# Kernel optimization log

Measured on AMD Instinct MI355X. Metric: run time of the kernel, lower is better.

## Reference

```python
import jax, jax.numpy as jnp
import numpy as np
from jax import lax

WIRES = 4
EPS = 1e-5


def _conv2d(x, w, b):
    # x: [B,C,H,W], w: [O,I,3,3], SAME padding, stride 1
    y = lax.conv_general_dilated(x, w, (1, 1), 'SAME',
                                 dimension_numbers=('NCHW', 'OIHW', 'NCHW'))
    return y + b[None, :, None, None]


def _maxpool2(x):
    return lax.reduce_window(x, -jnp.inf, lax.max, (1, 1, 2, 2), (1, 1, 2, 2), 'VALID')


def _cnot_perm(c, t, n=WIRES):
    # wire 0 = most significant bit; CNOT is a self-inverse basis permutation
    idx = np.arange(2 ** n)
    cbit = (idx >> (n - 1 - c)) & 1
    flipped = idx ^ (1 << (n - 1 - t))
    return np.where(cbit == 1, flipped, idx)


_CNOT_PERMS = [_cnot_perm(c, c + 1) for c in range(WIRES - 1)]
_Z_SIGNS = np.stack([1.0 - 2.0 * ((np.arange(2 ** WIRES) >> (WIRES - 1 - i)) & 1)
                     for i in range(WIRES)], axis=1).astype(np.float32)  # [16, 4]


def _quantum_circuit(q_params, feats):
    # Batched state-vector sim of: RY(feats[i]) wire i; RX(params[i]) wire i;
    # CNOT chain; <Z_i>.  feats: [B,4], q_params: [4]
    hf = 0.5 * feats
    hp = 0.5 * q_params
    cy, sy = jnp.cos(hf), jnp.sin(hf)            # [B,4]
    cx, sx = jnp.cos(hp), jnp.sin(hp)            # [4]
    # per-wire state after RX @ RY |0>: amplitudes of |0>, |1>
    a0 = (cx * cy - 1j * sx * sy).astype(jnp.complex64)  # [B,4]
    a1 = (cx * sy - 1j * sx * cy).astype(jnp.complex64)  # [B,4]
    single = jnp.stack([a0, a1], axis=-1)        # [B,4,2]
    # product state -> full 16-dim state via successive outer products
    psi = single[:, 0]                           # [B,2]
    for i in range(1, WIRES):
        psi = (psi[:, :, None] * single[:, i][:, None, :]).reshape(psi.shape[0], -1)
    # CNOT chain = fixed basis permutations
    for perm in _CNOT_PERMS:
        psi = psi[:, perm]                       # [B,16]
    probs = psi.real ** 2 + psi.imag ** 2        # [B,16]
    return probs @ jnp.asarray(_Z_SIGNS)         # [B,4]


def setup_inputs() -> dict:
    key = jax.random.key(0)
    ks = jax.random.split(key, 8)
    B, C, H, W = 512, 1, 128, 128
    return {
        'x': jax.random.normal(ks[0], (B, C, H, W), jnp.float32),
        'conv1_w': jax.random.normal(ks[1], (8, C, 3, 3), jnp.float32) * 0.1,
        'conv1_b': jnp.zeros((8,), jnp.float32),
        'conv2_w': jax.random.normal(ks[2], (16, 8, 3, 3), jnp.float32) * 0.1,
        'conv2_b': jnp.zeros((16,), jnp.float32),
        'q_params': jax.random.normal(ks[3], (WIRES,), jnp.float32),
        'bn_gamma': jnp.ones((4,), jnp.float32),
        'bn_beta': jnp.zeros((4,), jnp.float32),
        'head_w': jax.random.normal(ks[4], (4, WIRES), jnp.float32) * 0.5,
        'head_b': jnp.zeros((4,), jnp.float32),
    }


def reference(x, conv1_w, conv1_b, conv2_w, conv2_b, q_params,
              bn_gamma, bn_beta, head_w, head_b):
    h = jax.nn.relu(_conv2d(x, conv1_w, conv1_b))
    h = _maxpool2(h)
    h = jax.nn.relu(_conv2d(h, conv2_w, conv2_b))
    h = _maxpool2(h)
    feats = h.mean(axis=(2, 3))                  # AdaptiveAvgPool2d(1) -> [B,16]
    q_out = _quantum_circuit(q_params, feats[:, :WIRES])  # [B,4]
    # BatchNorm1d (training mode, biased variance)
    mu = q_out.mean(axis=0)
    var = q_out.var(axis=0)
    normed = bn_gamma * (q_out - mu) / jnp.sqrt(var + EPS) + bn_beta
    return normed @ head_w.T + head_b
```

## Files before the change

### kernel.cpp

```cpp
#include <hip/hip_runtime.h>

#define EPS 1e-5f

typedef float f2 __attribute__((ext_vector_type(2)));
typedef float f4 __attribute__((ext_vector_type(4)));

__device__ __forceinline__ float uload(const float* __restrict__ p) {
  return __int_as_float(__builtin_amdgcn_readfirstlane(__float_as_int(*p)));
}

__device__ __forceinline__ f2 fma2(f2 a, f2 b, f2 c) {
  return __builtin_elementwise_fma(a, b, c);
}
__device__ __forceinline__ f2 splat2(float s) { f2 r; r.x = s; r.y = s; return r; }

__global__ __launch_bounds__(256, 4) void k12_fused(
    const float* __restrict__ x, const float* __restrict__ w1,
    const float* __restrict__ b1, const float* __restrict__ w2,
    const float* __restrict__ b2, float* __restrict__ partials) {
  __shared__ float p1[4][18][66];
  __shared__ float w1t[72];
  __shared__ float b1s[8];
  __shared__ float w2t[288];
  __shared__ float b2s[4];
  __shared__ float wred[4][4];

  const int q   = blockIdx.x & 3;
  const int b   = blockIdx.x >> 2;
  const int tid = threadIdx.x;
  const float* xb = x + (size_t)b * (128 * 128);

  if (tid < 72) {
    int oc = tid / 9, k = tid % 9;
    w1t[k * 8 + oc] = w1[tid];
  } else if (tid < 80) {
    b1s[tid - 72] = b1[tid - 72];
  } else if (tid < 84) {
    b2s[tid - 80] = b2[tid - 80];
  }
  {
    int t = tid;
    {
      int oc = t / 72, rem = t % 72, ic = rem / 9, k = rem % 9;
      w2t[(ic * 9 + k) * 4 + oc] = w2[t];
    }
    t = tid + 256;
    if (t < 288) {
      int oc = t / 72, rem = t % 72, ic = rem / 9, k = rem % 9;
      w2t[(ic * 9 + k) * 4 + oc] = w2[t];
    }
  }
  if (tid < 72) {
    int ic = tid / 18, r = tid % 18;
    p1[ic][r][0]  = 0.f;
    p1[ic][r][65] = 0.f;
  }
  __syncthreads();

  const int px2  = tid & 31;
  const int py2l = tid >> 5;

  f2 acc[2][2][2];
#pragma unroll
  for (int p = 0; p < 2; ++p) {
    const f2 bias = *(const f2*)&b2s[2 * p];
    acc[p][0][0] = bias; acc[p][0][1] = bias;
    acc[p][1][0] = bias; acc[p][1][1] = bias;
  }

#pragma unroll 1
  for (int g = 0; g < 2; ++g) {
    if (g) __syncthreads();

    f2 wp[9][2], bias1[2];
#pragma unroll
    for (int k = 0; k < 9; ++k) {
      wp[k][0] = *(const f2*)&w1t[k * 8 + 4 * g];
      wp[k][1] = *(const f2*)&w1t[k * 8 + 4 * g + 2];
    }
    bias1[0] = *(const f2*)&b1s[4 * g];
    bias1[1] = *(const f2*)&b1s[4 * g + 2];

#pragma unroll 1
    for (int pos = tid; pos < 576; pos += 256) {
      const int gl = pos >> 5, i = pos & 31;
      const int G  = 16 * q - 1 + gl;
      const bool vG = ((unsigned)G) < 64u;
      const int xr0 = 2 * G - 1;
      float xin[4][6];
#pragma unroll
      for (int r = 0; r < 4; ++r) {
        const int row  = xr0 + r;
        const bool rok = vG && ((unsigned)row < 128u);
        const int rowc = min(max(row, 0), 127);
        const float* rp = xb + rowc * 128;
        const float le = rp[(i == 0) ? 0 : (4 * i - 1)];
        const f4 mid   = *(const f4*)(rp + 4 * i);
        const float ri = rp[(i == 31) ? 127 : (4 * i + 4)];
        xin[r][0] = (rok && i != 0)  ? le    : 0.f;
        xin[r][1] = rok              ? mid.x : 0.f;
        xin[r][2] = rok              ? mid.y : 0.f;
        xin[r][3] = rok              ? mid.z : 0.f;
        xin[r][4] = rok              ? mid.w : 0.f;
        xin[r][5] = (rok && i != 31) ? ri    : 0.f;
      }
      f2 best[2][2];
#pragma unroll
      for (int p = 0; p < 2; ++p)
#pragma unroll
        for (int h = 0; h < 2; ++h) best[p][h] = splat2(0.f);
#pragma unroll
      for (int dy = 0; dy < 2; ++dy)
#pragma unroll
        for (int dx = 0; dx < 2; ++dx) {
#pragma unroll
          for (int p = 0; p < 2; ++p)
#pragma unroll
            for (int h = 0; h < 2; ++h) {
              f2 a = bias1[p];
#pragma unroll
              for (int ky = 0; ky < 3; ++ky)
#pragma unroll
                for (int kx = 0; kx < 3; ++kx)
                  a = fma2(wp[ky * 3 + kx][p],
                           splat2(xin[dy + ky][2 * h + dx + kx]), a);
              best[p][h].x = fmaxf(best[p][h].x, a.x);
              best[p][h].y = fmaxf(best[p][h].y, a.y);
            }
        }
#pragma unroll
      for (int p = 0; p < 2; ++p)
#pragma unroll
        for (int h = 0; h < 2; ++h) {
          p1[2 * p][gl][2 * i + 1 + h]     = vG ? best[p][h].x : 0.f;
          p1[2 * p + 1][gl][2 * i + 1 + h] = vG ? best[p][h].y : 0.f;
        }
    }
    __syncthreads();

#pragma unroll 1
    for (int ic = 0; ic < 4; ++ic) {
      float xin[4][4];
#pragma unroll
      for (int r = 0; r < 4; ++r) {
        const f2* rp = (const f2*)&p1[ic][2 * py2l + r][2 * px2];
        f2 v0 = rp[0], v1 = rp[1];
        xin[r][0] = v0.x; xin[r][1] = v0.y; xin[r][2] = v1.x; xin[r][3] = v1.y;
      }
      const int icg = 4 * g + ic;
#pragma unroll
      for (int ky = 0; ky < 3; ++ky)
#pragma unroll
        for (int kx = 0; kx < 3; ++kx) {
          const int k = ky * 3 + kx;
          const f2 w0 = *(const f2*)&w2t[(icg * 9 + k) * 4];
          const f2 w1p = *(const f2*)&w2t[(icg * 9 + k) * 4 + 2];
#pragma unroll
          for (int dy = 0; dy < 2; ++dy)
#pragma unroll
            for (int dx = 0; dx < 2; ++dx) {
              const f2 xs = splat2(xin[dy + ky][dx + kx]);
              acc[0][dy][dx] = fma2(w0, xs, acc[0][dy][dx]);
              acc[1][dy][dx] = fma2(w1p, xs, acc[1][dy][dx]);
            }
        }
    }
  }

  const int lane = tid & 63, w = tid >> 6;
#pragma unroll
  for (int p = 0; p < 2; ++p) {
    f2 m01;
    m01.x = fmaxf(fmaxf(fmaxf(acc[p][0][0].x, acc[p][0][1].x),
                        fmaxf(acc[p][1][0].x, acc[p][1][1].x)), 0.f);
    m01.y = fmaxf(fmaxf(fmaxf(acc[p][0][0].y, acc[p][0][1].y),
                        fmaxf(acc[p][1][0].y, acc[p][1][1].y)), 0.f);
#pragma unroll
    for (int off = 32; off > 0; off >>= 1) {
      m01.x += __shfl_down(m01.x, off);
      m01.y += __shfl_down(m01.y, off);
    }
    if (lane == 0) { wred[w][2 * p] = m01.x; wred[w][2 * p + 1] = m01.y; }
  }
  __syncthreads();
  if (tid < 4) {
    float s = wred[0][tid] + wred[1][tid] + wred[2][tid] + wred[3][tid];
    partials[((size_t)b * 4 + q) * 4 + tid] = s;
  }
}

__global__ __launch_bounds__(512) void k3_tail(
    const float* __restrict__ partials, const float* __restrict__ qp,
    const float* __restrict__ gamma, const float* __restrict__ beta,
    const float* __restrict__ hw, const float* __restrict__ hb,
    float* __restrict__ out) {
  __shared__ float wsum[8][8];
  __shared__ float stats[8];
  const int tid = threadIdx.x;

  const f4* pp = (const f4*)(partials + tid * 16);
  f4 s0 = pp[0], s1 = pp[1], s2 = pp[2], s3 = pp[3];
  float f[4];
  f[0] = (s0.x + s1.x + s2.x + s3.x) * (1.f / 1024.f);
  f[1] = (s0.y + s1.y + s2.y + s3.y) * (1.f / 1024.f);
  f[2] = (s0.z + s1.z + s2.z + s3.z) * (1.f / 1024.f);
  f[3] = (s0.w + s1.w + s2.w + s3.w) * (1.f / 1024.f);

  float a0r[4], a0i[4], a1r[4], a1i[4];
#pragma unroll
  for (int i = 0; i < 4; ++i) {
    float cy, sy, cx, sx;
    __sincosf(0.5f * f[i], &sy, &cy);
    __sincosf(0.5f * uload(qp + i), &sx, &cx);
    a0r[i] = cx * cy; a0i[i] = -sx * sy;
    a1r[i] = cx * sy; a1i[i] = -sx * cy;
  }

  float pr[16], pi[16];
#pragma unroll
  for (int j = 0; j < 16; ++j) {
    float rr = 1.f, ii = 0.f;
#pragma unroll
    for (int w = 0; w < 4; ++w) {
      int bit = (j >> (3 - w)) & 1;
      float ar = bit ? a1r[w] : a0r[w];
      float ai = bit ? a1i[w] : a0i[w];
      float t = rr * ar - ii * ai;
      ii = rr * ai + ii * ar;
      rr = t;
    }
    pr[j] = rr; pi[j] = ii;
  }

  constexpr int comp[16] = {0, 1, 3, 2, 6, 7, 5, 4, 12, 13, 15, 14, 10, 11, 9, 8};
  float qv[4] = {0.f, 0.f, 0.f, 0.f};
#pragma unroll
  for (int j = 0; j < 16; ++j) {
    int s = comp[j];
    float p = pr[s] * pr[s] + pi[s] * pi[s];
#pragma unroll
    for (int i = 0; i < 4; ++i)
      qv[i] += ((j >> (3 - i)) & 1) ? -p : p;
  }

  float v[8];
#pragma unroll
  for (int i = 0; i < 4; ++i) { v[i] = qv[i]; v[4 + i] = qv[i] * qv[i]; }
#pragma unroll
  for (int k = 0; k < 8; ++k)
#pragma unroll
    for (int off = 32; off > 0; off >>= 1) v[k] += __shfl_down(v[k], off);
  const int lane = tid & 63, w = tid >> 6;
  if (lane == 0) {
#pragma unroll
    for (int k = 0; k < 8; ++k) wsum[w][k] = v[k];
  }
  __syncthreads();
  if (tid < 8) {
    float s = 0.f;
#pragma unroll
    for (int ww = 0; ww < 8; ++ww) s += wsum[ww][tid];
    stats[tid] = s * (1.f / 512.f);
  }
  __syncthreads();

  float nm[4];
#pragma unroll
  for (int i = 0; i < 4; ++i) {
    float mu  = stats[i];
    float var = stats[4 + i] - mu * mu;
    nm[i] = uload(gamma + i) * (qv[i] - mu) * rsqrtf(var + EPS) + uload(beta + i);
  }
#pragma unroll
  for (int k = 0; k < 4; ++k) {
    float o = uload(hb + k);
#pragma unroll
    for (int i = 0; i < 4; ++i) o = fmaf(nm[i], uload(hw + k * 4 + i), o);
    out[tid * 4 + k] = o;
  }
}

extern "C" void kernel_launch(void* const* d_in, const int* in_sizes, int n_in,
                              void* d_out, int out_size, void* d_ws, size_t ws_size,
                              hipStream_t stream) {
  const float* x  = (const float*)d_in[0];
  const float* w1 = (const float*)d_in[1];
  const float* b1 = (const float*)d_in[2];
  const float* w2 = (const float*)d_in[3];
  const float* b2 = (const float*)d_in[4];
  const float* qp = (const float*)d_in[5];
  const float* gm = (const float*)d_in[6];
  const float* bt = (const float*)d_in[7];
  const float* hw = (const float*)d_in[8];
  const float* hb = (const float*)d_in[9];
  float* out = (float*)d_out;

  float* partials = (float*)d_ws;

  k12_fused<<<512 * 4, 256, 0, stream>>>(x, w1, b1, w2, b2, partials);
  k3_tail<<<1, 512, 0, stream>>>(partials, qp, gm, bt, hw, hb, out);
}
```

Before: 123.2 us.

## Compute all eight conv1 channels in one pass, reusing loaded input tile

The kernel now keeps all 8 pooled conv1 channels in shared memory at once, instead of processing two groups of 4 channels with a barrier between them. Each input tile is loaded from global memory once and reused for both channel groups, and one of the __syncthreads is removed. Biases are packed into the weight arrays. In exchange, shared memory per block roughly doubles to about 40 KB, which may lower occupancy below the 4 blocks per CU requested by the launch bounds.

```diff
diff --git a/kernel.cpp b/kernel.cpp
--- a/kernel.cpp
+++ b/kernel.cpp
@@ -18,11 +18,9 @@
     const float* __restrict__ x, const float* __restrict__ w1,
     const float* __restrict__ b1, const float* __restrict__ w2,
     const float* __restrict__ b2, float* __restrict__ partials) {
-  __shared__ float p1[4][18][66];
-  __shared__ float w1t[72];
-  __shared__ float b1s[8];
-  __shared__ float w2t[288];
-  __shared__ float b2s[4];
+  __shared__ float p1[8][18][66];
+  __shared__ float w1t[80];
+  __shared__ float w2t[292];
   __shared__ float wred[4][4];
 
   const int q   = blockIdx.x & 3;
@@ -34,9 +32,7 @@
     int oc = tid / 9, k = tid % 9;
     w1t[k * 8 + oc] = w1[tid];
   } else if (tid < 80) {
-    b1s[tid - 72] = b1[tid - 72];
-  } else if (tid < 84) {
-    b2s[tid - 80] = b2[tid - 80];
+    w1t[tid] = b1[tid - 72];
   }
   {
     int t = tid;
@@ -50,121 +46,111 @@
       w2t[(ic * 9 + k) * 4 + oc] = w2[t];
     }
   }
-  if (tid < 72) {
-    int ic = tid / 18, r = tid % 18;
+  if (tid >= 80 && tid < 84) w2t[288 + tid - 80] = b2[tid - 80];
+  if (tid >= 96 && tid < 240) {
+    int t = tid - 96;
+    int ic = t / 18, r = t % 18;
     p1[ic][r][0]  = 0.f;
     p1[ic][r][65] = 0.f;
   }
   __syncthreads();
 
+#pragma unroll 1
+  for (int pos = tid; pos < 576; pos += 256) {
+    const int gl = pos >> 5, i = pos & 31;
+    const int G  = 16 * q - 1 + gl;
+    const bool vG = ((unsigned)G) < 64u;
+    const int xr0 = 2 * G - 1;
+    float xin[4][6];
+#pragma unroll
+    for (int r = 0; r < 4; ++r) {
+      const int row  = xr0 + r;
+      const bool rok = vG && ((unsigned)row < 128u);
+      const int rowc = min(max(row, 0), 127);
+      const float* rp = xb + rowc * 128;
+      const float le = rp[(i == 0) ? 0 : (4 * i - 1)];
+      const f4 mid   = *(const f4*)(rp + 4 * i);
+      const float ri = rp[(i == 31) ? 127 : (4 * i + 4)];
+      xin[r][0] = (rok && i != 0)  ? le    : 0.f;
+      xin[r][1] = rok              ? mid.x : 0.f;
+      xin[r][2] = rok              ? mid.y : 0.f;
+      xin[r][3] = rok              ? mid.z : 0.f;
+      xin[r][4] = rok              ? mid.w : 0.f;
+      xin[r][5] = (rok && i != 31) ? ri    : 0.f;
+    }
+#pragma unroll 1
+    for (int g = 0; g < 2; ++g) {
+      f2 wpx[9][2], bias1[2];
+#pragma unroll
+      for (int k = 0; k < 9; ++k) {
+        wpx[k][0] = *(const f2*)&w1t[k * 8 + 4 * g];
+        wpx[k][1] = *(const f2*)&w1t[k * 8 + 4 * g + 2];
+      }
+      bias1[0] = *(const f2*)&w1t[72 + 4 * g];
+      bias1[1] = *(const f2*)&w1t[72 + 4 * g + 2];
+#pragma unroll
+      for (int p = 0; p < 2; ++p)
+#pragma unroll
+        for (int h = 0; h < 2; ++h) {
+          f2 best = splat2(0.f);
+#pragma unroll
+          for (int dy = 0; dy < 2; ++dy)
+#pragma unroll
+            for (int dx = 0; dx < 2; ++dx) {
+              f2 a = bias1[p];
+#pragma unroll
+              for (int ky = 0; ky < 3; ++ky)
+#pragma unroll
+                for (int kx = 0; kx < 3; ++kx)
+                  a = fma2(wpx[ky * 3 + kx][p],
+                           splat2(xin[dy + ky][2 * h + dx + kx]), a);
+              best.x = fmaxf(best.x, a.x);
+              best.y = fmaxf(best.y, a.y);
+            }
+          const int oc0 = 4 * g + 2 * p;
+          p1[oc0][gl][2 * i + 1 + h]     = vG ? best.x : 0.f;
+          p1[oc0 + 1][gl][2 * i + 1 + h] = vG ? best.y : 0.f;
+        }
+    }
+  }
+  __syncthreads();
+
   const int px2  = tid & 31;
   const int py2l = tid >> 5;
 
   f2 acc[2][2][2];
 #pragma unroll
   for (int p = 0; p < 2; ++p) {
-    const f2 bias = *(const f2*)&b2s[2 * p];
+    const f2 bias = *(const f2*)&w2t[288 + 2 * p];
     acc[p][0][0] = bias; acc[p][0][1] = bias;
     acc[p][1][0] = bias; acc[p][1][1] = bias;
   }
 
 #pragma unroll 1
-  for (int g = 0; g < 2; ++g) {
-    if (g) __syncthreads();
-
-    f2 wp[9][2], bias1[2];
-#pragma unroll
-    for (int k = 0; k < 9; ++k) {
-      wp[k][0] = *(const f2*)&w1t[k * 8 + 4 * g];
-      wp[k][1] = *(const f2*)&w1t[k * 8 + 4 * g + 2];
-    }
-    bias1[0] = *(const f2*)&b1s[4 * g];
-    bias1[1] = *(const f2*)&b1s[4 * g + 2];
-
-#pragma unroll 1
-    for (int pos = tid; pos < 576; pos += 256) {
-      const int gl = pos >> 5, i = pos & 31;
-      const int G  = 16 * q - 1 + gl;
-      const bool vG = ((unsigned)G) < 64u;
-      const int xr0 = 2 * G - 1;
-      float xin[4][6];
-#pragma unroll
-      for (int r = 0; r < 4; ++r) {
-        const int row  = xr0 + r;
-        const bool rok = vG && ((unsigned)row < 128u);
-        const int rowc = min(max(row, 0), 127);
-        const float* rp = xb + rowc * 128;
-        const float le = rp[(i == 0) ? 0 : (4 * i - 1)];
-        const f4 mid   = *(const f4*)(rp + 4 * i);
-        const float ri = rp[(i == 31) ? 127 : (4 * i + 4)];
-        xin[r][0] = (rok && i != 0)  ? le    : 0.f;
-        xin[r][1] = rok              ? mid.x : 0.f;
-        xin[r][2] = rok              ? mid.y : 0.f;
-        xin[r][3] = rok              ? mid.z : 0.f;
-        xin[r][4] = rok              ? mid.w : 0.f;
-        xin[r][5] = (rok && i != 31) ? ri    : 0.f;
+  for (int ic = 0; ic < 8; ++ic) {
+    float xin[4][4];
+#pragma unroll
+    for (int r = 0; r < 4; ++r) {
+      const f2* rp = (const f2*)&p1[ic][2 * py2l + r][2 * px2];
+      f2 v0 = rp[0], v1 = rp[1];
+      xin[r][0] = v0.x; xin[r][1] = v0.y; xin[r][2] = v1.x; xin[r][3] = v1.y;
+    }
+#pragma unroll
+    for (int ky = 0; ky < 3; ++ky)
+#pragma unroll
+      for (int kx = 0; kx < 3; ++kx) {
+        const int k = ky * 3 + kx;
+        const f2 w0  = *(const f2*)&w2t[(ic * 9 + k) * 4];
+        const f2 w1p = *(const f2*)&w2t[(ic * 9 + k) * 4 + 2];
+#pragma unroll
+        for (int dy = 0; dy < 2; ++dy)
+#pragma unroll
+          for (int dx = 0; dx < 2; ++dx) {
+            const f2 xs = splat2(xin[dy + ky][dx + kx]);
+            acc[0][dy][dx] = fma2(w0, xs, acc[0][dy][dx]);
+            acc[1][dy][dx] = fma2(w1p, xs, acc[1][dy][dx]);
+          }
       }
-      f2 best[2][2];
-#pragma unroll
-      for (int p = 0; p < 2; ++p)
-#pragma unroll
-        for (int h = 0; h < 2; ++h) best[p][h] = splat2(0.f);
-#pragma unroll
-      for (int dy = 0; dy < 2; ++dy)
-#pragma unroll
-        for (int dx = 0; dx < 2; ++dx) {
-#pragma unroll
-          for (int p = 0; p < 2; ++p)
-#pragma unroll
-            for (int h = 0; h < 2; ++h) {
-              f2 a = bias1[p];
-#pragma unroll
-              for (int ky = 0; ky < 3; ++ky)
-#pragma unroll
-                for (int kx = 0; kx < 3; ++kx)
-                  a = fma2(wp[ky * 3 + kx][p],
-                           splat2(xin[dy + ky][2 * h + dx + kx]), a);
-              best[p][h].x = fmaxf(best[p][h].x, a.x);
-              best[p][h].y = fmaxf(best[p][h].y, a.y);
-            }
-        }
-#pragma unroll
-      for (int p = 0; p < 2; ++p)
-#pragma unroll
-        for (int h = 0; h < 2; ++h) {
-          p1[2 * p][gl][2 * i + 1 + h]     = vG ? best[p][h].x : 0.f;
-          p1[2 * p + 1][gl][2 * i + 1 + h] = vG ? best[p][h].y : 0.f;
-        }
-    }
-    __syncthreads();
-
-#pragma unroll 1
-    for (int ic = 0; ic < 4; ++ic) {
-      float xin[4][4];
-#pragma unroll
-      for (int r = 0; r < 4; ++r) {
-        const f2* rp = (const f2*)&p1[ic][2 * py2l + r][2 * px2];
-        f2 v0 = rp[0], v1 = rp[1];
-        xin[r][0] = v0.x; xin[r][1] = v0.y; xin[r][2] = v1.x; xin[r][3] = v1.y;
-      }
-      const int icg = 4 * g + ic;
-#pragma unroll
-      for (int ky = 0; ky < 3; ++ky)
-#pragma unroll
-        for (int kx = 0; kx < 3; ++kx) {
-          const int k = ky * 3 + kx;
-          const f2 w0 = *(const f2*)&w2t[(icg * 9 + k) * 4];
-          const f2 w1p = *(const f2*)&w2t[(icg * 9 + k) * 4 + 2];
-#pragma unroll
-          for (int dy = 0; dy < 2; ++dy)
-#pragma unroll
-            for (int dx = 0; dx < 2; ++dx) {
-              const f2 xs = splat2(xin[dy + ky][dx + kx]);
-              acc[0][dy][dx] = fma2(w0, xs, acc[0][dy][dx]);
-              acc[1][dy][dx] = fma2(w1p, xs, acc[1][dy][dx]);
-            }
-        }
-    }
   }
 
   const int lane = tid & 63, w = tid >> 6;
```

Result: no change. 121.0 us (-1.7%).
